# Kernel optimization log

Measured on AMD Instinct MI355X. Metric: run time of the kernel, lower is better.

Reference implementation:

```python
import jax, jax.numpy as jnp
import numpy as np
import math

B, L, H, NH = 2, 256, 512, 8
DH = H // NH


def setup_inputs() -> dict:
    key0 = jax.random.key(0)
    ks = jax.random.split(key0, 20)
    s = 0.02
    inp = {
        "key": jax.random.normal(ks[0], (B, L, H), jnp.float32),
        "query": jax.random.normal(ks[1], (B, L, H), jnp.float32),
        "value": jax.random.normal(ks[2], (B, L, H), jnp.float32),
        "seq_len": L // 2 + jax.random.randint(ks[3], (B,), 0, L // 2 + 1),
        "lex_num": 0,
        "pos_s": jax.random.randint(ks[4], (B, L), 0, L),
        "pos_e": jax.random.randint(ks[5], (B, L), 0, L),
        "rel_pos_embedding": jax.random.normal(ks[6], (B, L, L, H), jnp.float32),
        "Wk": jax.random.normal(ks[7], (H, H), jnp.float32) * s,
        "bk": jnp.zeros((H,), jnp.float32),
        "Wq": jax.random.normal(ks[8], (H, H), jnp.float32) * s,
        "bq": jnp.zeros((H,), jnp.float32),
        "Wv": jax.random.normal(ks[9], (H, H), jnp.float32) * s,
        "bv": jnp.zeros((H,), jnp.float32),
        "Wr": jax.random.normal(ks[10], (H, H), jnp.float32) * s,
        "br": jnp.zeros((H,), jnp.float32),
        "u": jax.random.normal(ks[11], (NH, DH), jnp.float32) * s,
        "v": jax.random.normal(ks[12], (NH, DH), jnp.float32) * s,
        "Wf": jax.random.normal(ks[13], (H, H), jnp.float32) * s,
        "bf": jnp.zeros((H,), jnp.float32),
    }
    return inp


def reference(key, query, value, seq_len, lex_num, pos_s, pos_e, rel_pos_embedding,
              Wk, bk, Wq, bq, Wv, bv, Wr, br, u, v, Wf, bf):
    b, sl = key.shape[0], key.shape[1]
    # projections (k/q/v/r_proj all True)
    k = key @ Wk + bk
    q = query @ Wq + bq
    val = value @ Wv + bv
    rel = rel_pos_embedding @ Wr + br            # [B,L,L,H]
    # split heads
    kh = k.reshape(b, sl, NH, DH).transpose(0, 2, 1, 3)    # [B,nh,L,dh]
    qh = q.reshape(b, sl, NH, DH).transpose(0, 2, 1, 3)
    vh = val.reshape(b, sl, NH, DH).transpose(0, 2, 1, 3)
    relh = rel.reshape(b, sl, sl, NH, DH)                   # [B,L,L,nh,dh]
    # A+C: (q + u) @ k^T
    q_u = qh + u[None, :, None, :]
    AC = jnp.einsum('bnid,bnjd->bnij', q_u, kh)
    # B+D: (q + v) . rel_pos per (i,j) pair
    q_v = qh + v[None, :, None, :]
    BD = jnp.einsum('bnid,bijnd->bnij', q_v, relh)
    scores = (AC + BD) / math.sqrt(DH)
    # mask padded keys: mask[b,j] = j < seq_len[b] + lex_num
    valid = jnp.arange(sl)[None, :] < (seq_len + lex_num)[:, None]   # [B,L]
    scores = jnp.where(valid[:, None, None, :], scores, -1e15)
    attn = jax.nn.softmax(scores, axis=-1)       # dropout p=0 -> identity
    out = jnp.einsum('bnij,bnjd->bnid', attn, vh)
    out = out.transpose(0, 2, 1, 3).reshape(b, sl, H)
    return out @ Wf + bf
```

## Files before the change

### kernel.cpp

```cpp
#include <hip/hip_runtime.h>
#include <math.h>


__global__ __launch_bounds__(256) void gemm512_k(
    const float* __restrict__ A0, const float* __restrict__ W0,
    const float* __restrict__ b0, float* __restrict__ C0,
    const float* __restrict__ A1, const float* __restrict__ W1,
    const float* __restrict__ b1, float* __restrict__ C1,
    const float* __restrict__ A2, const float* __restrict__ W2,
    const float* __restrict__ b2, float* __restrict__ C2) {
  const int z = blockIdx.z;
  const float* A    = (z == 0) ? A0 : (z == 1) ? A1 : A2;
  const float* W    = (z == 0) ? W0 : (z == 1) ? W1 : W2;
  const float* bias = (z == 0) ? b0 : (z == 1) ? b1 : b2;
  float* C          = (z == 0) ? C0 : (z == 1) ? C1 : C2;

  __shared__ float As[16][64];
  __shared__ float Bs[16][64];
  const int t  = threadIdx.x;
  const int tx = t & 15, ty = t >> 4;
  const int bm0 = blockIdx.y * 64, bn0 = blockIdx.x * 64;
  const int lm  = t >> 2;
  const int lkq = (t & 3) << 2;
  const int lk  = t >> 4;
  const int lnq = (t & 15) << 2;

  float acc[4][4] = {};
  float4 a4 = *(const float4*)&A[(bm0 + lm) * 512 + lkq];
  float4 b4 = *(const float4*)&W[lk * 512 + bn0 + lnq];
  for (int kt = 0; kt < 32; ++kt) {
    As[lkq + 0][lm] = a4.x;
    As[lkq + 1][lm] = a4.y;
    As[lkq + 2][lm] = a4.z;
    As[lkq + 3][lm] = a4.w;
    *(float4*)&Bs[lk][lnq] = b4;
    __syncthreads();
    float4 a4n = a4, b4n = b4;
    if (kt < 31) {
      a4n = *(const float4*)&A[(bm0 + lm) * 512 + (kt + 1) * 16 + lkq];
      b4n = *(const float4*)&W[((kt + 1) * 16 + lk) * 512 + bn0 + lnq];
    }
#pragma unroll
    for (int k = 0; k < 16; ++k) {
      float4 av = *(const float4*)&As[k][ty * 4];
      float4 bv = *(const float4*)&Bs[k][tx * 4];
      acc[0][0] = fmaf(av.x, bv.x, acc[0][0]);
      acc[0][1] = fmaf(av.x, bv.y, acc[0][1]);
      acc[0][2] = fmaf(av.x, bv.z, acc[0][2]);
      acc[0][3] = fmaf(av.x, bv.w, acc[0][3]);
      acc[1][0] = fmaf(av.y, bv.x, acc[1][0]);
      acc[1][1] = fmaf(av.y, bv.y, acc[1][1]);
      acc[1][2] = fmaf(av.y, bv.z, acc[1][2]);
      acc[1][3] = fmaf(av.y, bv.w, acc[1][3]);
      acc[2][0] = fmaf(av.z, bv.x, acc[2][0]);
      acc[2][1] = fmaf(av.z, bv.y, acc[2][1]);
      acc[2][2] = fmaf(av.z, bv.z, acc[2][2]);
      acc[2][3] = fmaf(av.z, bv.w, acc[2][3]);
      acc[3][0] = fmaf(av.w, bv.x, acc[3][0]);
      acc[3][1] = fmaf(av.w, bv.y, acc[3][1]);
      acc[3][2] = fmaf(av.w, bv.z, acc[3][2]);
      acc[3][3] = fmaf(av.w, bv.w, acc[3][3]);
    }
    __syncthreads();
    a4 = a4n;
    b4 = b4n;
  }
  float4 bb = *(const float4*)&bias[bn0 + tx * 4];
#pragma unroll
  for (int r = 0; r < 4; ++r) {
    float4 o;
    o.x = acc[r][0] + bb.x;
    o.y = acc[r][1] + bb.y;
    o.z = acc[r][2] + bb.z;
    o.w = acc[r][3] + bb.w;
    *(float4*)&C[(size_t)(bm0 + ty * 4 + r) * 512 + bn0 + tx * 4] = o;
  }
}

__global__ __launch_bounds__(256) void g_gemm_k(const float* __restrict__ q,
                                                const float* __restrict__ vbias,
                                                const float* __restrict__ Wr,
                                                float* __restrict__ g) {
  __shared__ float As[64][64];
  __shared__ float Bs[64][64];
  const int t   = threadIdx.x;
  const int bi0 = blockIdx.x * 64;
  const int eb  = blockIdx.y * 64;
  const int n   = blockIdx.z;
  const int row = t >> 2;
  const int dq  = (t & 3) << 4;
#pragma unroll
  for (int s = 0; s < 4; ++s) {
    int d = dq + s * 4;
    float4 a4 = *(const float4*)&q[(size_t)(bi0 + row) * 512 + n * 64 + d];
    float4 v4 = *(const float4*)&vbias[n * 64 + d];
    As[d + 0][row] = a4.x + v4.x;
    As[d + 1][row] = a4.y + v4.y;
    As[d + 2][row] = a4.z + v4.z;
    As[d + 3][row] = a4.w + v4.w;
    float4 b4 = *(const float4*)&Wr[(size_t)(eb + row) * 512 + n * 64 + d];
    Bs[d + 0][row] = b4.x;
    Bs[d + 1][row] = b4.y;
    Bs[d + 2][row] = b4.z;
    Bs[d + 3][row] = b4.w;
  }
  __syncthreads();
  const int tx = t & 15, ty = t >> 4;
  float acc[4][4] = {};
#pragma unroll 8
  for (int d = 0; d < 64; ++d) {
    float4 av = *(const float4*)&As[d][ty * 4];
    float4 bv = *(const float4*)&Bs[d][tx * 4];
    acc[0][0] = fmaf(av.x, bv.x, acc[0][0]);
    acc[0][1] = fmaf(av.x, bv.y, acc[0][1]);
    acc[0][2] = fmaf(av.x, bv.z, acc[0][2]);
    acc[0][3] = fmaf(av.x, bv.w, acc[0][3]);
    acc[1][0] = fmaf(av.y, bv.x, acc[1][0]);
    acc[1][1] = fmaf(av.y, bv.y, acc[1][1]);
    acc[1][2] = fmaf(av.y, bv.z, acc[1][2]);
    acc[1][3] = fmaf(av.y, bv.w, acc[1][3]);
    acc[2][0] = fmaf(av.z, bv.x, acc[2][0]);
    acc[2][1] = fmaf(av.z, bv.y, acc[2][1]);
    acc[2][2] = fmaf(av.z, bv.z, acc[2][2]);
    acc[2][3] = fmaf(av.z, bv.w, acc[2][3]);
    acc[3][0] = fmaf(av.w, bv.x, acc[3][0]);
    acc[3][1] = fmaf(av.w, bv.y, acc[3][1]);
    acc[3][2] = fmaf(av.w, bv.z, acc[3][2]);
    acc[3][3] = fmaf(av.w, bv.w, acc[3][3]);
  }
#pragma unroll
  for (int r = 0; r < 4; ++r) {
    float4 o = {acc[r][0], acc[r][1], acc[r][2], acc[r][3]};
    *(float4*)&g[((size_t)(bi0 + ty * 4 + r) * 8 + n) * 512 + eb + tx * 4] = o;
  }
}

__global__ __launch_bounds__(256) void attn_k(
    const float* __restrict__ q, const float* __restrict__ kk,
    const float* __restrict__ g, const float* __restrict__ rpe,
    const float* __restrict__ u, const float* __restrict__ v,
    const float* __restrict__ br, const int* __restrict__ seq_len,
    const int* __restrict__ lex_num, const float* __restrict__ val,
    float* __restrict__ ctx) {
  const int bi = blockIdx.x;
  const int b = bi >> 8;
  const int t = threadIdx.x;
  const int lane = t & 63, w = t >> 6;
  const int grp = lane >> 3, sub = lane & 7;
  const int e0 = lane << 3;
  __shared__ float sc[8][256];
  __shared__ float cterm[8];
  const int limit = seq_len[b] + lex_num[0];

  float qu[8];
  {
    const float* qrow = q + (size_t)bi * 512 + e0;
    float4 q0 = *(const float4*)qrow;
    float4 q1 = *(const float4*)(qrow + 4);
    float4 u0 = *(const float4*)(u + e0);
    float4 u1 = *(const float4*)(u + e0 + 4);
    qu[0] = q0.x + u0.x; qu[1] = q0.y + u0.y; qu[2] = q0.z + u0.z; qu[3] = q0.w + u0.w;
    qu[4] = q1.x + u1.x; qu[5] = q1.y + u1.y; qu[6] = q1.z + u1.z; qu[7] = q1.w + u1.w;
  }
  float gf[8][8];
#pragma unroll
  for (int n = 0; n < 8; ++n) {
    const float* grow = g + ((size_t)bi * 8 + n) * 512 + e0;
    float4 ga = *(const float4*)grow;
    float4 gb = *(const float4*)(grow + 4);
    gf[n][0] = ga.x; gf[n][1] = ga.y; gf[n][2] = ga.z; gf[n][3] = ga.w;
    gf[n][4] = gb.x; gf[n][5] = gb.y; gf[n][6] = gb.z; gf[n][7] = gb.w;
  }
  if (w == 0) {
    const float* qrow = q + (size_t)bi * 512 + e0;
    float4 q0 = *(const float4*)qrow;
    float4 q1 = *(const float4*)(qrow + 4);
    float4 v0 = *(const float4*)(v + e0);
    float4 v1 = *(const float4*)(v + e0 + 4);
    float4 r0 = *(const float4*)(br + e0);
    float4 r1 = *(const float4*)(br + e0 + 4);
    float p = (q0.x + v0.x) * r0.x;
    p = fmaf(q0.y + v0.y, r0.y, p);
    p = fmaf(q0.z + v0.z, r0.z, p);
    p = fmaf(q0.w + v0.w, r0.w, p);
    p = fmaf(q1.x + v1.x, r1.x, p);
    p = fmaf(q1.y + v1.y, r1.y, p);
    p = fmaf(q1.z + v1.z, r1.z, p);
    p = fmaf(q1.w + v1.w, r1.w, p);
    p += __shfl_xor(p, 1);
    p += __shfl_xor(p, 2);
    p += __shfl_xor(p, 4);
    if (sub == 0) cterm[grp] = p;
  }
  __syncthreads();

  const int s1 = sub & 1, s2 = (sub >> 1) & 1, s4 = (sub >> 2) & 1;
  const float* rbase = rpe + (size_t)bi * 256 * 512;
  const float* kbase = kk + (size_t)b * 256 * 512;
#pragma unroll 2
  for (int jj = 0; jj < 64; ++jj) {
    const int j = w * 64 + jj;
    const float* rrow = rbase + (size_t)j * 512 + e0;
    const float* krow = kbase + (size_t)j * 512 + e0;
    float4 r0 = *(const float4*)rrow;
    float4 r1 = *(const float4*)(rrow + 4);
    float4 k0 = *(const float4*)krow;
    float4 k1 = *(const float4*)(krow + 4);
    float kd = qu[0] * k0.x;
    kd = fmaf(qu[1], k0.y, kd);
    kd = fmaf(qu[2], k0.z, kd);
    kd = fmaf(qu[3], k0.w, kd);
    kd = fmaf(qu[4], k1.x, kd);
    kd = fmaf(qu[5], k1.y, kd);
    kd = fmaf(qu[6], k1.z, kd);
    kd = fmaf(qu[7], k1.w, kd);
    float a[8];
#pragma unroll
    for (int n = 0; n < 8; ++n) {
      float s = r0.x * gf[n][0];
      s = fmaf(r0.y, gf[n][1], s);
      s = fmaf(r0.z, gf[n][2], s);
      s = fmaf(r0.w, gf[n][3], s);
      s = fmaf(r1.x, gf[n][4], s);
      s = fmaf(r1.y, gf[n][5], s);
      s = fmaf(r1.z, gf[n][6], s);
      s = fmaf(r1.w, gf[n][7], s);
      a[n] = s + ((grp == n) ? kd : 0.0f);
    }
    float b0 = (s1 ? a[1] : a[0]) + __shfl_xor(s1 ? a[0] : a[1], 1);
    float b1 = (s1 ? a[3] : a[2]) + __shfl_xor(s1 ? a[2] : a[3], 1);
    float b2 = (s1 ? a[5] : a[4]) + __shfl_xor(s1 ? a[4] : a[5], 1);
    float b3 = (s1 ? a[7] : a[6]) + __shfl_xor(s1 ? a[6] : a[7], 1);
    float c0 = (s2 ? b1 : b0) + __shfl_xor(s2 ? b0 : b1, 2);
    float c1 = (s2 ? b3 : b2) + __shfl_xor(s2 ? b2 : b3, 2);
    float tot = (s4 ? c1 : c0) + __shfl_xor(s4 ? c0 : c1, 4);
    tot += __shfl_xor(tot, 8);
    tot += __shfl_xor(tot, 16);
    tot += __shfl_xor(tot, 32);
    if (lane < 8) {
      float sval = (tot + cterm[lane]) * 0.125f;
      if (j >= limit) sval = -1e15f;
      sc[lane][j] = sval;
    }
  }
  __syncthreads();

#pragma unroll
  for (int h = 0; h < 2; ++h) {
    const int n = w * 2 + h;
    float x0 = sc[n][lane], x1 = sc[n][lane + 64];
    float x2 = sc[n][lane + 128], x3 = sc[n][lane + 192];
    float m = fmaxf(fmaxf(x0, x1), fmaxf(x2, x3));
#pragma unroll
    for (int off = 1; off < 64; off <<= 1) m = fmaxf(m, __shfl_xor(m, off));
    float e0v = __expf(x0 - m), e1v = __expf(x1 - m);
    float e2v = __expf(x2 - m), e3v = __expf(x3 - m);
    float s = e0v + e1v + e2v + e3v;
#pragma unroll
    for (int off = 1; off < 64; off <<= 1) s += __shfl_xor(s, off);
    float inv = 1.0f / s;
    sc[n][lane] = e0v * inv;
    sc[n][lane + 64] = e1v * inv;
    sc[n][lane + 128] = e2v * inv;
    sc[n][lane + 192] = e3v * inv;
  }
  __syncthreads();

  const int c = t * 2;
  const int n = c >> 6;
  float2 acc = {0.f, 0.f};
  const float* vb = val + (size_t)b * 256 * 512 + c;
#pragma unroll 4
  for (int j = 0; j < 256; ++j) {
    float p = sc[n][j];
    float2 vv = *(const float2*)(vb + (size_t)j * 512);
    acc.x = fmaf(p, vv.x, acc.x);
    acc.y = fmaf(p, vv.y, acc.y);
  }
  float* crow = ctx + (size_t)bi * 512 + c;
  crow[0] = acc.x;
  crow[1] = acc.y;
}

extern "C" void kernel_launch(void* const* d_in, const int* in_sizes, int n_in,
                              void* d_out, int out_size, void* d_ws, size_t ws_size,
                              hipStream_t stream) {
  const float* key     = (const float*)d_in[0];
  const float* query   = (const float*)d_in[1];
  const float* value   = (const float*)d_in[2];
  const int* seq_len   = (const int*)d_in[3];
  const int* lex_num   = (const int*)d_in[4];
  const float* rpe     = (const float*)d_in[7];
  const float* Wk      = (const float*)d_in[8];
  const float* bk      = (const float*)d_in[9];
  const float* Wq      = (const float*)d_in[10];
  const float* bq      = (const float*)d_in[11];
  const float* Wv      = (const float*)d_in[12];
  const float* bv      = (const float*)d_in[13];
  const float* Wr      = (const float*)d_in[14];
  const float* br      = (const float*)d_in[15];
  const float* u       = (const float*)d_in[16];
  const float* v       = (const float*)d_in[17];
  const float* Wf      = (const float*)d_in[18];
  const float* bf      = (const float*)d_in[19];
  float* out = (float*)d_out;

  float* ws     = (float*)d_ws;
  float* q_ws   = ws;
  float* k_ws   = q_ws + 262144;
  float* val_ws = k_ws + 262144;
  float* g_ws   = val_ws + 262144;
  float* ctx_ws = g_ws + 2097152;

  dim3 blk(256);
  gemm512_k<<<dim3(8, 8, 3), blk, 0, stream>>>(query, Wq, bq, q_ws,
                                               key, Wk, bk, k_ws,
                                               value, Wv, bv, val_ws);
  g_gemm_k<<<dim3(8, 8, 8), blk, 0, stream>>>(q_ws, v, Wr, g_ws);
  attn_k<<<dim3(512), blk, 0, stream>>>(q_ws, k_ws, g_ws, rpe, u, v, br,
                                        seq_len, lex_num, val_ws, ctx_ws);
  gemm512_k<<<dim3(8, 8, 1), blk, 0, stream>>>(ctx_ws, Wf, bf, out,
                                               ctx_ws, Wf, bf, out,
                                               ctx_ws, Wf, bf, out);
}
```

Measured before the change: 475.4 us.

## Skip masked key positions in attention and retile projection GEMMs

The attention kernel now stops reading relative-position embeddings and values for key positions beyond the valid sequence length, writing the mask value directly instead. Blocks grow to 512 threads so each wave handles 32 keys and one head in softmax. The projection GEMM moves to 32x64 tiles with 128 threads to launch more blocks. The aim is to cut the dominant embedding bandwidth in proportion to padding, at the cost of load imbalance between waves.

```diff
diff --git a/kernel.cpp b/kernel.cpp
--- a/kernel.cpp
+++ b/kernel.cpp
@@ -2,7 +2,7 @@
 #include <math.h>
 
 
-__global__ __launch_bounds__(256) void gemm512_k(
+__global__ __launch_bounds__(128) void gemm512_k(
     const float* __restrict__ A0, const float* __restrict__ W0,
     const float* __restrict__ b0, float* __restrict__ C0,
     const float* __restrict__ A1, const float* __restrict__ W1,
@@ -15,30 +15,32 @@
   const float* bias = (z == 0) ? b0 : (z == 1) ? b1 : b2;
   float* C          = (z == 0) ? C0 : (z == 1) ? C1 : C2;
 
-  __shared__ float As[16][64];
+  __shared__ float As[16][32];
   __shared__ float Bs[16][64];
   const int t  = threadIdx.x;
   const int tx = t & 15, ty = t >> 4;
-  const int bm0 = blockIdx.y * 64, bn0 = blockIdx.x * 64;
-  const int lm  = t >> 2;
-  const int lkq = (t & 3) << 2;
-  const int lk  = t >> 4;
-  const int lnq = (t & 15) << 2;
+  const int bm0 = blockIdx.y * 32, bn0 = blockIdx.x * 64;
+  const int arow = t >> 2;
+  const int akq  = (t & 3) << 2;
+  const int bk   = t >> 4;
+  const int bnq  = (t & 15) << 2;
 
   float acc[4][4] = {};
-  float4 a4 = *(const float4*)&A[(bm0 + lm) * 512 + lkq];
-  float4 b4 = *(const float4*)&W[lk * 512 + bn0 + lnq];
+  float4 a4 = *(const float4*)&A[(bm0 + arow) * 512 + akq];
+  float4 w0 = *(const float4*)&W[bk * 512 + bn0 + bnq];
+  float4 w1 = *(const float4*)&W[(bk + 8) * 512 + bn0 + bnq];
   for (int kt = 0; kt < 32; ++kt) {
-    As[lkq + 0][lm] = a4.x;
-    As[lkq + 1][lm] = a4.y;
-    As[lkq + 2][lm] = a4.z;
-    As[lkq + 3][lm] = a4.w;
-    *(float4*)&Bs[lk][lnq] = b4;
+    As[akq + 0][arow] = a4.x;
+    As[akq + 1][arow] = a4.y;
+    As[akq + 2][arow] = a4.z;
+    As[akq + 3][arow] = a4.w;
+    *(float4*)&Bs[bk][bnq] = w0;
+    *(float4*)&Bs[bk + 8][bnq] = w1;
     __syncthreads();
-    float4 a4n = a4, b4n = b4;
     if (kt < 31) {
-      a4n = *(const float4*)&A[(bm0 + lm) * 512 + (kt + 1) * 16 + lkq];
-      b4n = *(const float4*)&W[((kt + 1) * 16 + lk) * 512 + bn0 + lnq];
+      a4 = *(const float4*)&A[(bm0 + arow) * 512 + (kt + 1) * 16 + akq];
+      w0 = *(const float4*)&W[((kt + 1) * 16 + bk) * 512 + bn0 + bnq];
+      w1 = *(const float4*)&W[((kt + 1) * 16 + bk + 8) * 512 + bn0 + bnq];
     }
 #pragma unroll
     for (int k = 0; k < 16; ++k) {
@@ -62,8 +64,6 @@
       acc[3][3] = fmaf(av.w, bv.w, acc[3][3]);
     }
     __syncthreads();
-    a4 = a4n;
-    b4 = b4n;
   }
   float4 bb = *(const float4*)&bias[bn0 + tx * 4];
 #pragma unroll
@@ -135,7 +135,7 @@
   }
 }
 
-__global__ __launch_bounds__(256) void attn_k(
+__global__ __launch_bounds__(512, 4) void attn_k(
     const float* __restrict__ q, const float* __restrict__ kk,
     const float* __restrict__ g, const float* __restrict__ rpe,
     const float* __restrict__ u, const float* __restrict__ v,
@@ -193,13 +193,21 @@
     if (sub == 0) cterm[grp] = p;
   }
   __syncthreads();
+  const float ct = (lane < 8) ? cterm[lane] : 0.0f;
+
+  const int jbase = w * 32;
+  int jend = limit - jbase;
+  jend = jend < 0 ? 0 : (jend > 32 ? 32 : jend);
+  if (lane < 8) {
+    for (int jj = jend; jj < 32; ++jj) sc[lane][jbase + jj] = -1e15f;
+  }
 
   const int s1 = sub & 1, s2 = (sub >> 1) & 1, s4 = (sub >> 2) & 1;
   const float* rbase = rpe + (size_t)bi * 256 * 512;
   const float* kbase = kk + (size_t)b * 256 * 512;
 #pragma unroll 2
-  for (int jj = 0; jj < 64; ++jj) {
-    const int j = w * 64 + jj;
+  for (int jj = 0; jj < jend; ++jj) {
+    const int j = jbase + jj;
     const float* rrow = rbase + (size_t)j * 512 + e0;
     const float* krow = kbase + (size_t)j * 512 + e0;
     float4 r0 = *(const float4*)rrow;
@@ -237,17 +245,12 @@
     tot += __shfl_xor(tot, 8);
     tot += __shfl_xor(tot, 16);
     tot += __shfl_xor(tot, 32);
-    if (lane < 8) {
-      float sval = (tot + cterm[lane]) * 0.125f;
-      if (j >= limit) sval = -1e15f;
-      sc[lane][j] = sval;
-    }
+    if (lane < 8) sc[lane][j] = (tot + ct) * 0.125f;
   }
   __syncthreads();
 
-#pragma unroll
-  for (int h = 0; h < 2; ++h) {
-    const int n = w * 2 + h;
+  {
+    const int n = w;
     float x0 = sc[n][lane], x1 = sc[n][lane + 64];
     float x2 = sc[n][lane + 128], x3 = sc[n][lane + 192];
     float m = fmaxf(fmaxf(x0, x1), fmaxf(x2, x3));
@@ -266,20 +269,15 @@
   }
   __syncthreads();
 
-  const int c = t * 2;
-  const int n = c >> 6;
-  float2 acc = {0.f, 0.f};
+  const int c = t;
+  const int n = t >> 6;
+  float acc = 0.0f;
   const float* vb = val + (size_t)b * 256 * 512 + c;
 #pragma unroll 4
-  for (int j = 0; j < 256; ++j) {
-    float p = sc[n][j];
-    float2 vv = *(const float2*)(vb + (size_t)j * 512);
-    acc.x = fmaf(p, vv.x, acc.x);
-    acc.y = fmaf(p, vv.y, acc.y);
-  }
-  float* crow = ctx + (size_t)bi * 512 + c;
-  crow[0] = acc.x;
-  crow[1] = acc.y;
+  for (int j = 0; j < limit; ++j) {
+    acc = fmaf(sc[n][j], vb[(size_t)j * 512], acc);
+  }
+  ctx[(size_t)bi * 512 + c] = acc;
 }
 
 extern "C" void kernel_launch(void* const* d_in, const int* in_sizes, int n_in,
@@ -312,14 +310,13 @@
   float* g_ws   = val_ws + 262144;
   float* ctx_ws = g_ws + 2097152;
 
-  dim3 blk(256);
-  gemm512_k<<<dim3(8, 8, 3), blk, 0, stream>>>(query, Wq, bq, q_ws,
-                                               key, Wk, bk, k_ws,
-                                               value, Wv, bv, val_ws);
-  g_gemm_k<<<dim3(8, 8, 8), blk, 0, stream>>>(q_ws, v, Wr, g_ws);
-  attn_k<<<dim3(512), blk, 0, stream>>>(q_ws, k_ws, g_ws, rpe, u, v, br,
-                                        seq_len, lex_num, val_ws, ctx_ws);
-  gemm512_k<<<dim3(8, 8, 1), blk, 0, stream>>>(ctx_ws, Wf, bf, out,
-                                               ctx_ws, Wf, bf, out,
-                                               ctx_ws, Wf, bf, out);
+  gemm512_k<<<dim3(8, 16, 3), dim3(128), 0, stream>>>(query, Wq, bq, q_ws,
+                                                      key, Wk, bk, k_ws,
+                                                      value, Wv, bv, val_ws);
+  g_gemm_k<<<dim3(8, 8, 8), dim3(256), 0, stream>>>(q_ws, v, Wr, g_ws);
+  attn_k<<<dim3(512), dim3(512), 0, stream>>>(q_ws, k_ws, g_ws, rpe, u, v, br,
+                                              seq_len, lex_num, val_ws, ctx_ws);
+  gemm512_k<<<dim3(8, 16, 1), dim3(128), 0, stream>>>(ctx_ws, Wf, bf, out,
+                                                      ctx_ws, Wf, bf, out,
+                                                      ctx_ws, Wf, bf, out);
 }
```

New measurement: 454.0 us. 1.05x faster.
